# Kernel optimization log

Hardware: AMD Instinct MI355X
Metric: run time of the kernel (lower is better)

Reference implementation:

```python
import jax, jax.numpy as jnp
import numpy as np

L, B, T, IN, D, H, FF, C = 6, 4, 1024, 256, 1024, 16, 4096, 10
HD = D // H
EPS = 1e-5


def _ln(x, g, b):
    mu = jnp.mean(x, axis=-1, keepdims=True)
    var = jnp.var(x, axis=-1, keepdims=True)
    return (x - mu) * jax.lax.rsqrt(var + EPS) * g + b


def setup_inputs() -> dict:
    key = jax.random.key(0)
    ks = jax.random.split(key, 10)
    s = 0.02
    rn = lambda k, shape: jax.random.normal(k, shape, jnp.float32) * s
    return {
        "x": jax.random.normal(ks[0], (B, T, IN), jnp.float32),
        "input_w": rn(ks[1], (D, IN)), "input_b": jnp.zeros((D,), jnp.float32),
        "Wqkv": rn(ks[2], (L, 3 * D, D)), "bqkv": jnp.zeros((L, 3 * D), jnp.float32),
        "Wo": rn(ks[3], (L, D, D)), "bo": jnp.zeros((L, D), jnp.float32),
        "ln1_g": jnp.ones((L, D), jnp.float32), "ln1_b": jnp.zeros((L, D), jnp.float32),
        "ln2_g": jnp.ones((L, D), jnp.float32), "ln2_b": jnp.zeros((L, D), jnp.float32),
        "W1": rn(ks[4], (L, FF, D)), "b1": jnp.zeros((L, FF), jnp.float32),
        "W2": rn(ks[5], (L, D, FF)), "b2": jnp.zeros((L, D), jnp.float32),
        "head_w": rn(ks[6], (C, D)), "head_b": jnp.zeros((C,), jnp.float32),
    }


def reference(x, input_w, input_b, Wqkv, bqkv, Wo, bo, ln1_g, ln1_b, ln2_g, ln2_b, W1, b1, W2, b2, head_w, head_b):
    Bx, Tx, _ = x.shape
    # input projection (torch Linear layout: [out,in])
    h = jnp.einsum('bti,di->btd', x, input_w) + input_b
    # ALiBi bias: mean slope across heads, additive |i-j| distance penalty
    slopes = 2.0 ** (-8.0 * jnp.arange(1, H + 1, dtype=jnp.float32) / H)
    slope = slopes.mean()
    idx = jnp.arange(Tx, dtype=jnp.float32)
    alibi = -slope * jnp.abs(idx[:, None] - idx[None, :])  # (T,T), same for every head
    scale = 1.0 / np.sqrt(HD)
    for l in range(L):
        qkv = jnp.einsum('btd,ed->bte', h, Wqkv[l]) + bqkv[l]
        q, k, v = jnp.split(qkv, 3, axis=-1)
        q = q.reshape(Bx, Tx, H, HD)
        k = k.reshape(Bx, Tx, H, HD)
        v = v.reshape(Bx, Tx, H, HD)
        scores = jnp.einsum('bthd,bshd->bhts', q, k) * scale + alibi
        attn = jax.nn.softmax(scores, axis=-1)
        o = jnp.einsum('bhts,bshd->bthd', attn, v).reshape(Bx, Tx, D)
        o = jnp.einsum('btd,ed->bte', o, Wo[l]) + bo[l]
        h = _ln(h + o, ln1_g[l], ln1_b[l])  # post-norm
        ff = jax.nn.relu(jnp.einsum('btd,fd->btf', h, W1[l]) + b1[l])
        ff = jnp.einsum('btf,df->btd', ff, W2[l]) + b2[l]
        h = _ln(h + ff, ln2_g[l], ln2_b[l])
    last = h[:, -1, :]
    return jnp.einsum('bd,cd->bc', last, head_w) + head_b
```

## Files before the change

kernel.cpp:

```cpp
#include <hip/hip_runtime.h>
#include <cmath>

#define D_MODEL 1024
#define N_HEADS 16
#define HEAD_DIM 64
#define SEQ 1024
#define BATCH 4
#define FF_DIM 4096
#define IN_DIM 256
#define N_LAYERS 6
#define N_CLS 10

typedef __bf16 bf16x8 __attribute__((ext_vector_type(8)));
typedef __bf16 bf16x4 __attribute__((ext_vector_type(4)));
typedef float f32x4 __attribute__((ext_vector_type(4)));
typedef unsigned short u16x8 __attribute__((ext_vector_type(8)));

__device__ __forceinline__ unsigned short f2bf(float f) {
    return __builtin_bit_cast(unsigned short, (__bf16)f);
}
__device__ __forceinline__ float bf2f(unsigned short u) {
    return __uint_as_float((unsigned int)u << 16);
}
__device__ __forceinline__ float fexp2(float x) {
    return __builtin_amdgcn_exp2f(x);
}

__device__ __forceinline__ void gll16(const void* g, void* l) {
    __builtin_amdgcn_global_load_lds((const __attribute__((address_space(1))) void*)g,
                                     (__attribute__((address_space(3))) void*)l, 16, 0, 0);
}

__global__ __launch_bounds__(256)
void cvt_f32_bf16(const float* __restrict__ src, unsigned short* __restrict__ dst, int n) {
    int i = (blockIdx.x * 256 + threadIdx.x) * 4;
    if (i + 4 <= n) {
        float4 v = *(const float4*)(src + i);
        ushort4 o;
        o.x = f2bf(v.x); o.y = f2bf(v.y); o.z = f2bf(v.z); o.w = f2bf(v.w);
        *(ushort4*)(dst + i) = o;
    }
}

#define WQKV_SZ (3 * D_MODEL * D_MODEL)
#define WO_SZ   (D_MODEL * D_MODEL)
#define W1_SZ   (FF_DIM * D_MODEL)
#define W2_SZ   (D_MODEL * FF_DIM)
__global__ __launch_bounds__(256)
void cvt_layer(const float* __restrict__ wq, const float* __restrict__ wo,
               const float* __restrict__ w1, const float* __restrict__ w2,
               unsigned short* __restrict__ dq, unsigned short* __restrict__ dvo,
               unsigned short* __restrict__ d1, unsigned short* __restrict__ d2)
{
    int i = (blockIdx.x * 256 + threadIdx.x) * 4;
    const float* s; unsigned short* d; int off;
    if (i < WQKV_SZ)                    { s = wq; d = dq;  off = i; }
    else if (i < WQKV_SZ + WO_SZ)       { s = wo; d = dvo; off = i - WQKV_SZ; }
    else if (i < WQKV_SZ + WO_SZ + W1_SZ) { s = w1; d = d1; off = i - WQKV_SZ - WO_SZ; }
    else                                { s = w2; d = d2;  off = i - WQKV_SZ - WO_SZ - W1_SZ; }
    float4 v = *(const float4*)(s + off);
    ushort4 o;
    o.x = f2bf(v.x); o.y = f2bf(v.y); o.z = f2bf(v.z); o.w = f2bf(v.w);
    *(ushort4*)(d + off) = o;
}

template<int MU, bool LOADB, bool GATE, typename F>
__device__ __forceinline__
void gphase(f32x4 (&acc)[8][4], bf16x8 (&bfr)[4],
            const unsigned short* slabA, const unsigned short* slabB,
            const int (&aoff)[2][4], const int (&boff)[4], F&& stage, bool gate0)
{
    bf16x8 afr[4];
    if (LOADB) {
        _Pragma("unroll")
        for (int n = 0; n < 4; ++n) bfr[n] = *(const bf16x8*)(slabB + boff[n]);
    }
    _Pragma("unroll")
    for (int m = 0; m < 4; ++m) afr[m] = *(const bf16x8*)(slabA + aoff[MU][m]);
    stage();
    __builtin_amdgcn_s_barrier();
    asm volatile("s_waitcnt lgkmcnt(0)" ::: "memory");
    __builtin_amdgcn_sched_barrier(0);
    __builtin_amdgcn_s_setprio(1);
    _Pragma("unroll")
    for (int m = 0; m < 4; ++m)
        _Pragma("unroll")
        for (int n = 0; n < 4; ++n)
            acc[MU * 4 + m][n] =
                __builtin_amdgcn_mfma_f32_16x16x32_bf16(afr[m], bfr[n], acc[MU * 4 + m][n], 0, 0, 0);
    __builtin_amdgcn_s_setprio(0);
    if (GATE) {
        if (gate0) asm volatile("s_waitcnt vmcnt(0)" ::: "memory");
        else       asm volatile("s_waitcnt vmcnt(4)" ::: "memory");
    }
    __builtin_amdgcn_s_barrier();
}

__global__ __launch_bounds__(512, 2)
void gemm256(const unsigned short* __restrict__ A, const unsigned short* __restrict__ B,
             const float* __restrict__ bias,
             float* __restrict__ Cf, unsigned short* __restrict__ Cb,
             int N, int lda, int klen, int relu, size_t slab_stride)
{
    extern __shared__ unsigned short lds[];
    auto slA = [&](int buf, int kh) { return lds + (buf * 2 + kh) * 8192; };
    auto slB = [&](int buf, int kh) { return lds + 32768 + (buf * 2 + kh) * 8192; };

    const int nbc = N >> 8;
    const int nwg = gridDim.x;
    const int orig = blockIdx.x;
    const int xcd = orig & 7, lid = orig >> 3;
    const int q = nwg >> 3, r = nwg & 7;
    const int wgid = (xcd < r ? xcd * (q + 1) : r * (q + 1) + (xcd - r) * q) + lid;
    const int brow = wgid / nbc, bcol = wgid % nbc;
    const int kpart = blockIdx.y;

    const int tid = threadIdx.x;
    const int w = tid >> 6, l = tid & 63;
    const int wr = w >> 2, wc = w & 3;
    const int lr = l & 15, lg4 = l >> 4;

    const unsigned short* Ab = A + (size_t)brow * 256 * lda + (size_t)kpart * klen;
    const unsigned short* Bb = B + (size_t)bcol * 256 * lda + (size_t)kpart * klen;
    float* Cfp = Cf;
    unsigned short* Cbp = Cb ? Cb + (size_t)kpart * slab_stride : nullptr;
    const float* biasp = (kpart == 0) ? bias : nullptr;

    const int G0 = w * 128 + l;
    const int tr0 = G0 >> 2;
    const int lg0 = (G0 & 3) ^ ((tr0 >> 1) & 3);

    auto stA = [&](int buf, int kh, int tile) {
        unsigned short* d = slA(buf, kh) + G0 * 8;
        const unsigned short* s = Ab + (size_t)tr0 * lda + tile * 64 + kh * 32 + lg0 * 8;
        gll16(s, d);
        gll16(s + (size_t)16 * lda, d + 512);
    };
    auto stB = [&](int buf, int kh, int tile) {
        unsigned short* d = slB(buf, kh) + G0 * 8;
        const unsigned short* s = Bb + (size_t)tr0 * lda + tile * 64 + kh * 32 + lg0 * 8;
        gll16(s, d);
        gll16(s + (size_t)16 * lda, d + 512);
    };

    int aoff[2][4], boff[4];
    #pragma unroll
    for (int mu = 0; mu < 2; ++mu)
        #pragma unroll
        for (int m = 0; m < 4; ++m) {
            int tA = wr * 128 + mu * 64 + m * 16 + lr;
            aoff[mu][m] = tA * 32 + ((lg4 ^ ((tA >> 1) & 3)) << 3);
        }
    #pragma unroll
    for (int n = 0; n < 4; ++n) {
        int tB = wc * 64 + n * 16 + lr;
        boff[n] = tB * 32 + ((lg4 ^ ((tB >> 1) & 3)) << 3);
    }

    f32x4 acc[8][4] = {};

    const int KT = klen >> 6;
    stA(0, 0, 0); stA(0, 1, 0); stB(0, 0, 0); stB(0, 1, 0);
    if (KT > 1) { stA(1, 0, 1); stA(1, 1, 1); stB(1, 0, 1); stB(1, 1, 1); }
    asm volatile("s_waitcnt vmcnt(0)" ::: "memory");
    __builtin_amdgcn_s_barrier();

    for (int I = 0; I < KT / 2; ++I) {
        const int t2 = 2 * I;
        const bool s12 = (I > 0);
        const bool more = (t2 + 2 < KT);
        bf16x8 bfr[4];
        gphase<0, true , false>(acc, bfr, slA(0,0), slB(0,0), aoff, boff, [&]{ if (s12)  stA(1,1,t2+1); }, false);
        gphase<1, false, false>(acc, bfr, slA(0,0), slB(0,0), aoff, boff, [&]{ if (s12)  stB(1,1,t2+1); }, false);
        gphase<0, true , false>(acc, bfr, slA(0,1), slB(0,1), aoff, boff, [&]{ if (more) stA(0,0,t2+2); }, false);
        gphase<1, false, true >(acc, bfr, slA(0,1), slB(0,1), aoff, boff, [&]{ if (more) stB(0,0,t2+2); }, !more);
        gphase<0, true , false>(acc, bfr, slA(1,0), slB(1,0), aoff, boff, [&]{ if (more) stA(0,1,t2+2); }, false);
        gphase<1, false, false>(acc, bfr, slA(1,0), slB(1,0), aoff, boff, [&]{ if (more) stB(0,1,t2+2); }, false);
        gphase<0, true , false>(acc, bfr, slA(1,1), slB(1,1), aoff, boff, [&]{ if (more) stA(1,0,t2+3); }, false);
        gphase<1, false, true >(acc, bfr, slA(1,1), slB(1,1), aoff, boff, [&]{ if (more) stB(1,0,t2+3); }, !more);
    }

    const int crow0 = brow * 256 + wr * 128;
    const int ccol0 = bcol * 256 + wc * 64;
    #pragma unroll
    for (int n = 0; n < 4; ++n) {
        int col = ccol0 + n * 16 + lr;
        float bv = biasp ? biasp[col] : 0.0f;
        #pragma unroll
        for (int m = 0; m < 8; ++m) {
            int row0 = crow0 + m * 16 + lg4 * 4;
            size_t base_i = (size_t)row0 * N + col;
            #pragma unroll
            for (int j = 0; j < 4; ++j) {
                float v = acc[m][n][j] + bv;
                if (relu) v = fmaxf(v, 0.0f);
                size_t idx = base_i + (size_t)j * N;
                if (Cfp) Cfp[idx] = v;
                if (Cbp) Cbp[idx] = f2bf(v);
            }
        }
    }
}

__global__ __launch_bounds__(256, 3)
void attn_alibi(const unsigned short* __restrict__ qkv,
                unsigned short* __restrict__ out,
                float slope2)
{
    const int bid = blockIdx.x;
    const int id = (bid & 7) * 128 + (bid >> 3);
    const int qt = id & 15;
    const int bh = id >> 4;
    const int h  = bh & (N_HEADS - 1);
    const int b  = bh >> 4;
    const int w  = threadIdx.x >> 6, l = threadIdx.x & 63;
    const int lr = l & 15, lg = l >> 4;

    __shared__ __align__(16) unsigned short lsK[2][64 * 64];
    __shared__ __align__(16) unsigned short lsVt[2][64 * 64];
    __shared__ __align__(16) unsigned short lsP[4 * 16 * 64];

    const size_t rs = 3 * D_MODEL;
    const unsigned short* base = qkv + (size_t)b * SEQ * rs;
    const int qrow_w = qt * 64 + w * 16;
    const float c1 = 0.125f * 1.4426950408889634f;

    bf16x8 aq[2];
    #pragma unroll
    for (int ks = 0; ks < 2; ++ks)
        aq[ks] = *(const bf16x8*)(base + (size_t)(qrow_w + lr) * rs + h * HEAD_DIM + ks * 32 + lg * 8);

    float m_run = -1e30f, s_run = 0.f;
    f32x4 oacc[4] = {};
    const float qi = (float)(qrow_w + lr);

    auto stageK = [&](int buf, int kt) {
        #pragma unroll
        for (int i = 0; i < 2; ++i) {
            int chunk = i * 4 + w;
            int e = chunk * 512 + l * 8;
            int row = e >> 6, c = e & 63;
            int gcol = c ^ ((row & 7) << 3);
            gll16(base + (size_t)(kt * 64 + row) * rs + D_MODEL + h * HEAD_DIM + gcol,
                  &lsK[buf][chunk * 512]);
        }
    };
    auto stageV = [&](int buf, int kt) {
        #pragma unroll
        for (int i = 0; i < 2; ++i) {
            int oct = i * 4 + w;
            int kj  = l;
            u16x8 v = *(const u16x8*)(base + (size_t)(kt * 64 + kj) * rs + 2 * D_MODEL + h * HEAD_DIM + oct * 8);
            #pragma unroll
            for (int jj = 0; jj < 8; ++jj) {
                int row = oct * 8 + jj;
                lsVt[buf][row * 64 + (kj ^ ((row & 7) << 3))] = v[jj];
            }
        }
    };

    const int p_lo = max(0, (qt - 2) >> 1);
    const int p_hi = min(SEQ / 128, ((qt + 2) >> 1) + 1);

    for (int p = p_lo; p < p_hi; ++p) {
        const int kt0 = 2 * p;
        stageK(0, kt0); stageK(1, kt0 + 1);
        stageV(0, kt0); stageV(1, kt0 + 1);
        __syncthreads();

        f32x4 s0[4] = {}, s1[4] = {};
        __builtin_amdgcn_s_setprio(1);
        #pragma unroll
        for (int ks = 0; ks < 2; ++ks) {
            #pragma unroll
            for (int n = 0; n < 4; ++n) {
                int row = n * 16 + lr;
                int co = (ks * 32 + lg * 8) ^ ((row & 7) << 3);
                bf16x8 bk0 = *(const bf16x8*)&lsK[0][row * 64 + co];
                bf16x8 bk1 = *(const bf16x8*)&lsK[1][row * 64 + co];
                s0[n] = __builtin_amdgcn_mfma_f32_16x16x32_bf16(bk0, aq[ks], s0[n], 0, 0, 0);
                s1[n] = __builtin_amdgcn_mfma_f32_16x16x32_bf16(bk1, aq[ks], s1[n], 0, 0, 0);
            }
        }
        __builtin_amdgcn_s_setprio(0);

        float mx = -1e30f;
        #pragma unroll
        for (int n = 0; n < 4; ++n)
            #pragma unroll
            for (int jj = 0; jj < 4; ++jj) {
                float k0f = (float)(kt0 * 64 + n * 16 + lg * 4 + jj);
                float v0 = fmaf(s0[n][jj], c1, -slope2 * fabsf(qi - k0f));
                float v1 = fmaf(s1[n][jj], c1, -slope2 * fabsf(qi - k0f - 64.0f));
                s0[n][jj] = v0;
                s1[n][jj] = v1;
                mx = fmaxf(mx, fmaxf(v0, v1));
            }
        mx = fmaxf(mx, __shfl_xor(mx, 16));
        mx = fmaxf(mx, __shfl_xor(mx, 32));
        if (__any(mx > m_run + 8.0f)) {
            float mnew = fmaxf(m_run, mx);
            float corr = fexp2(m_run - mnew);
            m_run = mnew;
            s_run *= corr;
            #pragma unroll
            for (int j = 0; j < 4; ++j) {
                float cj = __shfl(corr, lg * 4 + j);
                #pragma unroll
                for (int nd = 0; nd < 4; ++nd)
                    oacc[nd][j] *= cj;
            }
        }
        float psum = 0.f;
        #pragma unroll
        for (int n = 0; n < 4; ++n)
            #pragma unroll
            for (int jj = 0; jj < 4; ++jj) {
                float p0 = fexp2(s0[n][jj] - m_run);
                float p1 = fexp2(s1[n][jj] - m_run);
                s0[n][jj] = p0;
                s1[n][jj] = p1;
                psum += p0 + p1;
            }
        psum += __shfl_xor(psum, 16);
        psum += __shfl_xor(psum, 32);
        s_run += psum;

        #pragma unroll
        for (int t = 0; t < 2; ++t) {
            #pragma unroll
            for (int n = 0; n < 4; ++n) {
                f32x4 sv = t ? s1[n] : s0[n];
                bf16x4 pk;
                pk[0] = (__bf16)sv[0]; pk[1] = (__bf16)sv[1];
                pk[2] = (__bf16)sv[2]; pk[3] = (__bf16)sv[3];
                *(bf16x4*)&lsP[w * 1024 + lr * 64 + ((n * 16 + lg * 4) ^ ((lr & 7) << 3))] = pk;
            }
            __builtin_amdgcn_s_setprio(1);
            #pragma unroll
            for (int ks = 0; ks < 2; ++ks) {
                bf16x8 ap = *(const bf16x8*)&lsP[w * 1024 + lr * 64 + ((ks * 32 + lg * 8) ^ ((lr & 7) << 3))];
                #pragma unroll
                for (int nd = 0; nd < 4; ++nd) {
                    int row = nd * 16 + lr;
                    bf16x8 bv = *(const bf16x8*)&lsVt[t][row * 64 + ((ks * 32 + lg * 8) ^ ((row & 7) << 3))];
                    oacc[nd] = __builtin_amdgcn_mfma_f32_16x16x32_bf16(ap, bv, oacc[nd], 0, 0, 0);
                }
            }
            __builtin_amdgcn_s_setprio(0);
        }
        __syncthreads();
    }

    float inv = 1.0f / s_run;
    #pragma unroll
    for (int j = 0; j < 4; ++j) {
        float invj = __shfl(inv, lg * 4 + j);
        int qrow = qrow_w + lg * 4 + j;
        #pragma unroll
        for (int nd = 0; nd < 4; ++nd) {
            int d = nd * 16 + lr;
            out[((size_t)b * SEQ + qrow) * D_MODEL + h * HEAD_DIM + d] = f2bf(oacc[nd][j] * invj);
        }
    }
}

__global__ __launch_bounds__(256)
void add_ln(const unsigned short* __restrict__ resid, const unsigned short* __restrict__ delta,
            size_t slab, int nslab,
            const float* __restrict__ g, const float* __restrict__ beta,
            unsigned short* __restrict__ out_b)
{
    const int w = threadIdx.x >> 6, l = threadIdx.x & 63;
    const int row = blockIdx.x * 4 + w;
    const size_t off0 = (size_t)row * D_MODEL + l * 8;

    float x[16];
    #pragma unroll
    for (int c = 0; c < 2; ++c) {
        u16x8 rv = *(const u16x8*)(resid + off0 + c * 512);
        #pragma unroll
        for (int j = 0; j < 8; ++j) x[c * 8 + j] = bf2f(rv[j]);
    }
    for (int p = 0; p < nslab; ++p) {
        #pragma unroll
        for (int c = 0; c < 2; ++c) {
            u16x8 dv = *(const u16x8*)(delta + p * slab + off0 + c * 512);
            #pragma unroll
            for (int j = 0; j < 8; ++j) x[c * 8 + j] += bf2f(dv[j]);
        }
    }
    float s = 0.f, s2 = 0.f;
    #pragma unroll
    for (int i = 0; i < 16; ++i) { s += x[i]; s2 += x[i] * x[i]; }
    #pragma unroll
    for (int d = 1; d < 64; d <<= 1) {
        s  += __shfl_xor(s, d);
        s2 += __shfl_xor(s2, d);
    }
    float mu  = s * (1.0f / D_MODEL);
    float var = s2 * (1.0f / D_MODEL) - mu * mu;
    float rsq = rsqrtf(var + 1e-5f);

    #pragma unroll
    for (int c = 0; c < 2; ++c) {
        int e0 = l * 8 + c * 512;
        float4 g0 = *(const float4*)(g + e0);
        float4 g1 = *(const float4*)(g + e0 + 4);
        float4 b0 = *(const float4*)(beta + e0);
        float4 b1 = *(const float4*)(beta + e0 + 4);
        float gv[8] = {g0.x, g0.y, g0.z, g0.w, g1.x, g1.y, g1.z, g1.w};
        float bv[8] = {b0.x, b0.y, b0.z, b0.w, b1.x, b1.y, b1.z, b1.w};
        u16x8 ov;
        #pragma unroll
        for (int j = 0; j < 8; ++j)
            ov[j] = f2bf((x[c * 8 + j] - mu) * rsq * gv[j] + bv[j]);
        *(u16x8*)(out_b + off0 + c * 512) = ov;
    }
}

__global__ __launch_bounds__(256)
void head_kernel(const unsigned short* __restrict__ h, const float* __restrict__ hw,
                 const float* __restrict__ hb, float* __restrict__ out)
{
    const int wv = threadIdx.x >> 6, l = threadIdx.x & 63;
    const int c = blockIdx.x;
    const unsigned short* hr = h + ((size_t)wv * SEQ + (SEQ - 1)) * D_MODEL;
    const float* wc = hw + (size_t)c * D_MODEL;
    float s = 0.f;
    #pragma unroll
    for (int i = 0; i < 16; ++i) {
        int k = i * 64 + l;
        s += bf2f(hr[k]) * wc[k];
    }
    #pragma unroll
    for (int d = 1; d < 64; d <<= 1)
        s += __shfl_xor(s, d);
    if (l == 0) out[wv * N_CLS + c] = s + hb[c];
}

extern "C" void kernel_launch(void* const* d_in, const int* in_sizes, int n_in,
                              void* d_out, int out_size, void* d_ws, size_t ws_size,
                              hipStream_t stream)
{
    const float* x     = (const float*)d_in[0];
    const float* in_w  = (const float*)d_in[1];
    const float* in_b  = (const float*)d_in[2];
    const float* Wqkv  = (const float*)d_in[3];
    const float* bqkv  = (const float*)d_in[4];
    const float* Wo    = (const float*)d_in[5];
    const float* bo    = (const float*)d_in[6];
    const float* ln1g  = (const float*)d_in[7];
    const float* ln1b  = (const float*)d_in[8];
    const float* ln2g  = (const float*)d_in[9];
    const float* ln2b  = (const float*)d_in[10];
    const float* W1    = (const float*)d_in[11];
    const float* b1    = (const float*)d_in[12];
    const float* W2    = (const float*)d_in[13];
    const float* b2    = (const float*)d_in[14];
    const float* headw = (const float*)d_in[15];
    const float* headb = (const float*)d_in[16];
    float* out = (float*)d_out;

    (void)hipFuncSetAttribute((const void*)gemm256, hipFuncAttributeMaxDynamicSharedMemorySize, 131072);

    char* ws = (char*)d_ws;
    size_t off = 0;
    auto alloc = [&](size_t bytes) -> void* {
        void* p = ws + off;
        off += (bytes + 255) & ~(size_t)255;
        return p;
    };
    const int MT = BATCH * SEQ;
    const size_t SLAB = (size_t)MT * D_MODEL;

    unsigned short* x_bf   = (unsigned short*)alloc((size_t)MT * IN_DIM * 2);
    unsigned short* h_bf   = (unsigned short*)alloc(SLAB * 2);
    unsigned short* qkv_bf = (unsigned short*)alloc((size_t)MT * 3 * D_MODEL * 2);
    unsigned short* att_bf = (unsigned short*)alloc(SLAB * 2);
    unsigned short* ff_bf  = (unsigned short*)alloc((size_t)MT * FF_DIM * 2);
    unsigned short* tmp_bf = (unsigned short*)alloc(SLAB * 2 * 4);
    unsigned short* win_bf = (unsigned short*)alloc((size_t)D_MODEL * IN_DIM * 2);
    unsigned short* wq_bf  = (unsigned short*)alloc((size_t)WQKV_SZ * 2);
    unsigned short* wo_bf  = (unsigned short*)alloc((size_t)WO_SZ * 2);
    unsigned short* w1_bf  = (unsigned short*)alloc((size_t)W1_SZ * 2);
    unsigned short* w2_bf  = (unsigned short*)alloc((size_t)W2_SZ * 2);

    double ssum = 0.0;
    for (int i = 1; i <= N_HEADS; ++i) ssum += pow(2.0, -8.0 * i / N_HEADS);
    const float slope = (float)(ssum / N_HEADS);
    const float slope2 = slope * 1.4426950408889634f;

    auto cvt = [&](const float* s, unsigned short* d, int n) {
        cvt_f32_bf16<<<n / 1024, 256, 0, stream>>>(s, d, n);
    };

    cvt(x, x_bf, MT * IN_DIM);
    cvt(in_w, win_bf, D_MODEL * IN_DIM);
    gemm256<<<dim3(16 * 4, 1), 512, 131072, stream>>>(
        x_bf, win_bf, in_b, nullptr, h_bf, D_MODEL, IN_DIM, IN_DIM, 0, 0);

    const int CVT_BLKS = (WQKV_SZ + WO_SZ + W1_SZ + W2_SZ) / 1024;

    for (int layer = 0; layer < N_LAYERS; ++layer) {
        cvt_layer<<<CVT_BLKS, 256, 0, stream>>>(
            Wqkv + (size_t)layer * WQKV_SZ, Wo + (size_t)layer * WO_SZ,
            W1 + (size_t)layer * W1_SZ, W2 + (size_t)layer * W2_SZ,
            wq_bf, wo_bf, w1_bf, w2_bf);

        gemm256<<<dim3(16 * 12, 1), 512, 131072, stream>>>(
            h_bf, wq_bf, bqkv + (size_t)layer * 3 * D_MODEL,
            nullptr, qkv_bf, 3 * D_MODEL, D_MODEL, D_MODEL, 0, 0);

        attn_alibi<<<BATCH * N_HEADS * (SEQ / 64), 256, 0, stream>>>(qkv_bf, att_bf, slope2);

        gemm256<<<dim3(16 * 4, 2), 512, 131072, stream>>>(
            att_bf, wo_bf, bo + (size_t)layer * D_MODEL,
            nullptr, tmp_bf, D_MODEL, D_MODEL, D_MODEL / 2, 0, SLAB);

        add_ln<<<MT / 4, 256, 0, stream>>>(h_bf, tmp_bf, SLAB, 2,
            ln1g + (size_t)layer * D_MODEL, ln1b + (size_t)layer * D_MODEL, h_bf);

        gemm256<<<dim3(16 * 16, 1), 512, 131072, stream>>>(
            h_bf, w1_bf, b1 + (size_t)layer * FF_DIM,
            nullptr, ff_bf, FF_DIM, D_MODEL, D_MODEL, 1, 0);

        gemm256<<<dim3(16 * 4, 4), 512, 131072, stream>>>(
            ff_bf, w2_bf, b2 + (size_t)layer * D_MODEL,
            nullptr, tmp_bf, D_MODEL, FF_DIM, FF_DIM / 4, 0, SLAB);

        add_ln<<<MT / 4, 256, 0, stream>>>(h_bf, tmp_bf, SLAB, 4,
            ln2g + (size_t)layer * D_MODEL, ln2b + (size_t)layer * D_MODEL, h_bf);
    }

    head_kernel<<<N_CLS, 256, 0, stream>>>(h_bf, headw, headb, out);
}
```

Measured before the change: 1.233 ms.

## Fuse fp32-to-bf16 weight conversion into GEMM B-operand loading

Removes the separate per-layer weight conversion kernels. The GEMM now streams fp32 weights straight into LDS through a three-slot ring buffer with a new swizzle, and converts them to bf16 when building the fragments. This drops one full pass that read fp32 weights and wrote bf16 copies. In exchange each GEMM moves twice the B-operand bytes, uses 160KB of LDS (occupancy drops to one block per CU), and restructures the K-loop pipeline and its wait counts.

```diff
diff --git a/kernel.cpp b/kernel.cpp
--- a/kernel.cpp
+++ b/kernel.cpp
@@ -42,38 +42,23 @@
     }
 }
 
-#define WQKV_SZ (3 * D_MODEL * D_MODEL)
-#define WO_SZ   (D_MODEL * D_MODEL)
-#define W1_SZ   (FF_DIM * D_MODEL)
-#define W2_SZ   (D_MODEL * FF_DIM)
-__global__ __launch_bounds__(256)
-void cvt_layer(const float* __restrict__ wq, const float* __restrict__ wo,
-               const float* __restrict__ w1, const float* __restrict__ w2,
-               unsigned short* __restrict__ dq, unsigned short* __restrict__ dvo,
-               unsigned short* __restrict__ d1, unsigned short* __restrict__ d2)
-{
-    int i = (blockIdx.x * 256 + threadIdx.x) * 4;
-    const float* s; unsigned short* d; int off;
-    if (i < WQKV_SZ)                    { s = wq; d = dq;  off = i; }
-    else if (i < WQKV_SZ + WO_SZ)       { s = wo; d = dvo; off = i - WQKV_SZ; }
-    else if (i < WQKV_SZ + WO_SZ + W1_SZ) { s = w1; d = d1; off = i - WQKV_SZ - WO_SZ; }
-    else                                { s = w2; d = d2;  off = i - WQKV_SZ - WO_SZ - W1_SZ; }
-    float4 v = *(const float4*)(s + off);
-    ushort4 o;
-    o.x = f2bf(v.x); o.y = f2bf(v.y); o.z = f2bf(v.z); o.w = f2bf(v.w);
-    *(ushort4*)(d + off) = o;
-}
-
 template<int MU, bool LOADB, bool GATE, typename F>
 __device__ __forceinline__
 void gphase(f32x4 (&acc)[8][4], bf16x8 (&bfr)[4],
-            const unsigned short* slabA, const unsigned short* slabB,
-            const int (&aoff)[2][4], const int (&boff)[4], F&& stage, bool gate0)
+            const unsigned short* slabA, const float* slabB,
+            const int (&aoff)[2][4], const int (&boffB)[4][2], F&& stage, bool gate0)
 {
     bf16x8 afr[4];
     if (LOADB) {
         _Pragma("unroll")
-        for (int n = 0; n < 4; ++n) bfr[n] = *(const bf16x8*)(slabB + boff[n]);
+        for (int n = 0; n < 4; ++n) {
+            f32x4 lo = *(const f32x4*)(slabB + boffB[n][0]);
+            f32x4 hi = *(const f32x4*)(slabB + boffB[n][1]);
+            bf16x8 r;
+            _Pragma("unroll")
+            for (int j = 0; j < 4; ++j) { r[j] = (__bf16)lo[j]; r[4 + j] = (__bf16)hi[j]; }
+            bfr[n] = r;
+        }
     }
     _Pragma("unroll")
     for (int m = 0; m < 4; ++m) afr[m] = *(const bf16x8*)(slabA + aoff[MU][m]);
@@ -91,20 +76,20 @@
     __builtin_amdgcn_s_setprio(0);
     if (GATE) {
         if (gate0) asm volatile("s_waitcnt vmcnt(0)" ::: "memory");
-        else       asm volatile("s_waitcnt vmcnt(4)" ::: "memory");
+        else       asm volatile("s_waitcnt vmcnt(6)" ::: "memory");
     }
     __builtin_amdgcn_s_barrier();
 }
 
-__global__ __launch_bounds__(512, 2)
-void gemm256(const unsigned short* __restrict__ A, const unsigned short* __restrict__ B,
+__global__ __launch_bounds__(512, 1)
+void gemm256(const unsigned short* __restrict__ A, const float* __restrict__ B,
              const float* __restrict__ bias,
              float* __restrict__ Cf, unsigned short* __restrict__ Cb,
              int N, int lda, int klen, int relu, size_t slab_stride)
 {
     extern __shared__ unsigned short lds[];
-    auto slA = [&](int buf, int kh) { return lds + (buf * 2 + kh) * 8192; };
-    auto slB = [&](int buf, int kh) { return lds + 32768 + (buf * 2 + kh) * 8192; };
+    auto slA  = [&](int buf, int kh) { return lds + (buf * 2 + kh) * 8192; };
+    auto slBr = [&](int ring) { return (float*)(lds + 32768 + ring * 16384); };
 
     const int nbc = N >> 8;
     const int nwg = gridDim.x;
@@ -121,7 +106,7 @@
     const int lr = l & 15, lg4 = l >> 4;
 
     const unsigned short* Ab = A + (size_t)brow * 256 * lda + (size_t)kpart * klen;
-    const unsigned short* Bb = B + (size_t)bcol * 256 * lda + (size_t)kpart * klen;
+    const float*          Bb = B + (size_t)bcol * 256 * lda + (size_t)kpart * klen;
     float* Cfp = Cf;
     unsigned short* Cbp = Cb ? Cb + (size_t)kpart * slab_stride : nullptr;
     const float* biasp = (kpart == 0) ? bias : nullptr;
@@ -136,14 +121,19 @@
         gll16(s, d);
         gll16(s + (size_t)16 * lda, d + 512);
     };
-    auto stB = [&](int buf, int kh, int tile) {
-        unsigned short* d = slB(buf, kh) + G0 * 8;
-        const unsigned short* s = Bb + (size_t)tr0 * lda + tile * 64 + kh * 32 + lg0 * 8;
-        gll16(s, d);
-        gll16(s + (size_t)16 * lda, d + 512);
+    auto stB = [&](int ring, int kh, int tile) {
+        float* dst = slBr(ring);
+        const float* sb = Bb + tile * 64 + kh * 32;
+        #pragma unroll
+        for (int c = 0; c < 4; ++c) {
+            int G = tid + c * 512;
+            int row = G >> 3, gq = G & 7;
+            int ksrc = gq ^ (row & 7);
+            gll16(sb + (size_t)row * lda + ksrc * 4, dst + G * 4);
+        }
     };
 
-    int aoff[2][4], boff[4];
+    int aoff[2][4], boffB[4][2];
     #pragma unroll
     for (int mu = 0; mu < 2; ++mu)
         #pragma unroll
@@ -154,30 +144,32 @@
     #pragma unroll
     for (int n = 0; n < 4; ++n) {
         int tB = wc * 64 + n * 16 + lr;
-        boff[n] = tB * 32 + ((lg4 ^ ((tB >> 1) & 3)) << 3);
+        #pragma unroll
+        for (int c = 0; c < 2; ++c)
+            boffB[n][c] = tB * 32 + (((2 * lg4 + c) ^ (tB & 7)) << 2);
     }
 
     f32x4 acc[8][4] = {};
 
     const int KT = klen >> 6;
-    stA(0, 0, 0); stA(0, 1, 0); stB(0, 0, 0); stB(0, 1, 0);
-    if (KT > 1) { stA(1, 0, 1); stA(1, 1, 1); stB(1, 0, 1); stB(1, 1, 1); }
+    stA(0, 0, 0); stA(0, 1, 0);
+    stB(0, 0, 0); stB(1, 1, 0);
     asm volatile("s_waitcnt vmcnt(0)" ::: "memory");
     __builtin_amdgcn_s_barrier();
 
-    for (int I = 0; I < KT / 2; ++I) {
-        const int t2 = 2 * I;
-        const bool s12 = (I > 0);
-        const bool more = (t2 + 2 < KT);
+    for (int t = 0; t < KT; ++t) {
+        const int b = t & 1;
+        const bool more = (t + 1 < KT);
+        const int r0 = (2 * t) % 3, r1 = (2 * t + 1) % 3, r2 = (2 * t + 2) % 3;
         bf16x8 bfr[4];
-        gphase<0, true , false>(acc, bfr, slA(0,0), slB(0,0), aoff, boff, [&]{ if (s12)  stA(1,1,t2+1); }, false);
-        gphase<1, false, false>(acc, bfr, slA(0,0), slB(0,0), aoff, boff, [&]{ if (s12)  stB(1,1,t2+1); }, false);
-        gphase<0, true , false>(acc, bfr, slA(0,1), slB(0,1), aoff, boff, [&]{ if (more) stA(0,0,t2+2); }, false);
-        gphase<1, false, true >(acc, bfr, slA(0,1), slB(0,1), aoff, boff, [&]{ if (more) stB(0,0,t2+2); }, !more);
-        gphase<0, true , false>(acc, bfr, slA(1,0), slB(1,0), aoff, boff, [&]{ if (more) stA(0,1,t2+2); }, false);
-        gphase<1, false, false>(acc, bfr, slA(1,0), slB(1,0), aoff, boff, [&]{ if (more) stB(0,1,t2+2); }, false);
-        gphase<0, true , false>(acc, bfr, slA(1,1), slB(1,1), aoff, boff, [&]{ if (more) stA(1,0,t2+3); }, false);
-        gphase<1, false, true >(acc, bfr, slA(1,1), slB(1,1), aoff, boff, [&]{ if (more) stB(1,0,t2+3); }, !more);
+        gphase<0, true , false>(acc, bfr, slA(b, 0), slBr(r0), aoff, boffB,
+                                [&]{ if (more) stB(r2, 0, t + 1); }, false);
+        gphase<1, false, true >(acc, bfr, slA(b, 0), slBr(r0), aoff, boffB,
+                                [&]{ if (more) stA(b ^ 1, 0, t + 1); }, !more);
+        gphase<0, true , false>(acc, bfr, slA(b, 1), slBr(r1), aoff, boffB,
+                                [&]{ if (more) stB(r0, 1, t + 1); }, false);
+        gphase<1, false, true >(acc, bfr, slA(b, 1), slBr(r1), aoff, boffB,
+                                [&]{ if (more) stA(b ^ 1, 1, t + 1); }, !more);
     }
 
     const int crow0 = brow * 256 + wr * 128;
@@ -462,7 +454,7 @@
     const float* headb = (const float*)d_in[16];
     float* out = (float*)d_out;
 
-    (void)hipFuncSetAttribute((const void*)gemm256, hipFuncAttributeMaxDynamicSharedMemorySize, 131072);
+    (void)hipFuncSetAttribute((const void*)gemm256, hipFuncAttributeMaxDynamicSharedMemorySize, 163840);
 
     char* ws = (char*)d_ws;
     size_t off = 0;
@@ -473,6 +465,10 @@
     };
     const int MT = BATCH * SEQ;
     const size_t SLAB = (size_t)MT * D_MODEL;
+    const int WQKV_SZ = 3 * D_MODEL * D_MODEL;
+    const int WO_SZ   = D_MODEL * D_MODEL;
+    const int W1_SZ   = FF_DIM * D_MODEL;
+    const int W2_SZ   = D_MODEL * FF_DIM;
 
     unsigned short* x_bf   = (unsigned short*)alloc((size_t)MT * IN_DIM * 2);
     unsigned short* h_bf   = (unsigned short*)alloc(SLAB * 2);
@@ -480,53 +476,36 @@
     unsigned short* att_bf = (unsigned short*)alloc(SLAB * 2);
     unsigned short* ff_bf  = (unsigned short*)alloc((size_t)MT * FF_DIM * 2);
     unsigned short* tmp_bf = (unsigned short*)alloc(SLAB * 2 * 4);
-    unsigned short* win_bf = (unsigned short*)alloc((size_t)D_MODEL * IN_DIM * 2);
-    unsigned short* wq_bf  = (unsigned short*)alloc((size_t)WQKV_SZ * 2);
-    unsigned short* wo_bf  = (unsigned short*)alloc((size_t)WO_SZ * 2);
-    unsigned short* w1_bf  = (unsigned short*)alloc((size_t)W1_SZ * 2);
-    unsigned short* w2_bf  = (unsigned short*)alloc((size_t)W2_SZ * 2);
 
     double ssum = 0.0;
     for (int i = 1; i <= N_HEADS; ++i) ssum += pow(2.0, -8.0 * i / N_HEADS);
     const float slope = (float)(ssum / N_HEADS);
     const float slope2 = slope * 1.4426950408889634f;
 
-    auto cvt = [&](const float* s, unsigned short* d, int n) {
-        cvt_f32_bf16<<<n / 1024, 256, 0, stream>>>(s, d, n);
-    };
-
-    cvt(x, x_bf, MT * IN_DIM);
-    cvt(in_w, win_bf, D_MODEL * IN_DIM);
-    gemm256<<<dim3(16 * 4, 1), 512, 131072, stream>>>(
-        x_bf, win_bf, in_b, nullptr, h_bf, D_MODEL, IN_DIM, IN_DIM, 0, 0);
-
-    const int CVT_BLKS = (WQKV_SZ + WO_SZ + W1_SZ + W2_SZ) / 1024;
+    cvt_f32_bf16<<<(MT * IN_DIM) / 1024, 256, 0, stream>>>(x, x_bf, MT * IN_DIM);
+    gemm256<<<dim3(16 * 4, 1), 512, 163840, stream>>>(
+        x_bf, in_w, in_b, nullptr, h_bf, D_MODEL, IN_DIM, IN_DIM, 0, 0);
 
     for (int layer = 0; layer < N_LAYERS; ++layer) {
-        cvt_layer<<<CVT_BLKS, 256, 0, stream>>>(
-            Wqkv + (size_t)layer * WQKV_SZ, Wo + (size_t)layer * WO_SZ,
-            W1 + (size_t)layer * W1_SZ, W2 + (size_t)layer * W2_SZ,
-            wq_bf, wo_bf, w1_bf, w2_bf);
-
-        gemm256<<<dim3(16 * 12, 1), 512, 131072, stream>>>(
-            h_bf, wq_bf, bqkv + (size_t)layer * 3 * D_MODEL,
+        gemm256<<<dim3(16 * 12, 1), 512, 163840, stream>>>(
+            h_bf, Wqkv + (size_t)layer * WQKV_SZ, bqkv + (size_t)layer * 3 * D_MODEL,
             nullptr, qkv_bf, 3 * D_MODEL, D_MODEL, D_MODEL, 0, 0);
 
         attn_alibi<<<BATCH * N_HEADS * (SEQ / 64), 256, 0, stream>>>(qkv_bf, att_bf, slope2);
 
-        gemm256<<<dim3(16 * 4, 2), 512, 131072, stream>>>(
-            att_bf, wo_bf, bo + (size_t)layer * D_MODEL,
+        gemm256<<<dim3(16 * 4, 2), 512, 163840, stream>>>(
+            att_bf, Wo + (size_t)layer * WO_SZ, bo + (size_t)layer * D_MODEL,
             nullptr, tmp_bf, D_MODEL, D_MODEL, D_MODEL / 2, 0, SLAB);
 
         add_ln<<<MT / 4, 256, 0, stream>>>(h_bf, tmp_bf, SLAB, 2,
             ln1g + (size_t)layer * D_MODEL, ln1b + (size_t)layer * D_MODEL, h_bf);
 
-        gemm256<<<dim3(16 * 16, 1), 512, 131072, stream>>>(
-            h_bf, w1_bf, b1 + (size_t)layer * FF_DIM,
+        gemm256<<<dim3(16 * 16, 1), 512, 163840, stream>>>(
+            h_bf, W1 + (size_t)layer * W1_SZ, b1 + (size_t)layer * FF_DIM,
             nullptr, ff_bf, FF_DIM, D_MODEL, D_MODEL, 1, 0);
 
-        gemm256<<<dim3(16 * 4, 4), 512, 131072, stream>>>(
-            ff_bf, w2_bf, b2 + (size_t)layer * D_MODEL,
+        gemm256<<<dim3(16 * 4, 4), 512, 163840, stream>>>(
+            ff_bf, W2 + (size_t)layer * W2_SZ, b2 + (size_t)layer * D_MODEL,
             nullptr, tmp_bf, D_MODEL, FF_DIM, FF_DIM / 4, 0, SLAB);
 
         add_ln<<<MT / 4, 256, 0, stream>>>(h_bf, tmp_bf, SLAB, 4,
```

Result: slower. 1.377 ms (+11.7%).
